# Kernel tuning notes

Measured on AMD Instinct MI355X. Metric: run time of the kernel, lower is better.

The kernel has to match this reference:

```python
import jax, jax.numpy as jnp
import numpy as np

B, T, V, H, L = 2048, 128, 256, 20, 15  # batch, seq_len, vocab, hidden, max_label


def setup_inputs() -> dict:
    key = jax.random.key(0)
    ks = jax.random.split(key, 8)
    g = lambda k, shape, s: (jax.random.normal(k, shape, jnp.float32) * s)
    return {
        "x": jax.random.randint(ks[0], (B, T), 0, V, dtype=jnp.int32),
        "W0": g(ks[1], (V, 3 * H), 0.06),   # input kernel layer 0 [V, 3H] (z|r|h)
        "U0": g(ks[2], (H, 3 * H), 0.2),    # recurrent kernel layer 0
        "b0i": jnp.zeros((3 * H,), jnp.float32),  # input bias (reset_after=True split bias)
        "b0r": jnp.zeros((3 * H,), jnp.float32),  # recurrent bias
        "W1": g(ks[3], (H, 3 * H), 0.2),
        "U1": g(ks[4], (H, 3 * H), 0.2),
        "b1i": jnp.zeros((3 * H,), jnp.float32),
        "b1r": jnp.zeros((3 * H,), jnp.float32),
        "Wd": g(ks[5], (H, L), 0.2),
        "bd": jnp.zeros((L,), jnp.float32),
        "drop_rate": 0,  # identity dropout (deterministic reference)
    }


def _gru_cell(h, xw, U, br):
    # Keras GRUCell with reset_after=True:
    #   xw = x @ W + b_in  (precomputed), rec = h @ U + b_rec
    rec = h @ U + br
    xz, xr, xh = jnp.split(xw, 3, axis=-1)
    rz, rr, rh = jnp.split(rec, 3, axis=-1)
    z = jax.nn.sigmoid(xz + rz)
    r = jax.nn.sigmoid(xr + rr)
    hh = jnp.tanh(xh + r * rh)
    return z * h + (1.0 - z) * hh


def reference(x, W0, U0, b0i, b0r, W1, U1, b1i, b1r, Wd, bd, drop_rate):
    # one_hot(x) @ W0 == gather rows of W0 (same math, no [B,T,V] materialization)
    xW0 = W0[x] + b0i                 # [B, T, 3H]
    xW0 = jnp.swapaxes(xW0, 0, 1)     # [T, B, 3H] for scan over time

    def step(carry, xw_t):
        h0, h1 = carry
        h0 = _gru_cell(h0, xw_t, U0, b0r)
        xw1 = h0 @ W1 + b1i
        h1 = _gru_cell(h1, xw1, U1, b1r)
        return (h0, h1), None

    h0 = jnp.zeros((x.shape[0], H), W0.dtype)
    h1 = jnp.zeros((x.shape[0], H), W0.dtype)
    (h0, h1), _ = jax.lax.scan(step, (h0, h1), xW0)
    # tf.nn.dropout with rate 0 is the identity
    out = h1
    logits = jax.nn.softmax(out @ Wd + bd, axis=-1)  # [B, L]
    return logits
```

## Files before the change

### kernel.cpp

```cpp
#include <hip/hip_runtime.h>


#define BB 2048
#define TT 128
#define HH 20
#define LL 15
#define H3 60

typedef float v2f __attribute__((ext_vector_type(2)));

__device__ __forceinline__ float bclane(float v, int k) {
    return __int_as_float(__builtin_amdgcn_readlane(__float_as_int(v), k));
}
__device__ __forceinline__ float dpp_rshr1(float v) {
    return __int_as_float(__builtin_amdgcn_update_dpp(
        0, __float_as_int(v), 0x111, 0xF, 0xF, true));
}
__device__ __forceinline__ float fast_rcp(float x) { return __builtin_amdgcn_rcpf(x); }
__device__ __forceinline__ float sigm(float x) { return fast_rcp(1.f + __expf(-x)); }
__device__ __forceinline__ float tanh_f(float x) { return 1.f - 2.f * fast_rcp(1.f + __expf(2.f * x)); }
#define PIN(v) asm volatile("" : "+v"(v))
#define LDSFENCE() asm volatile("" ::: "memory")

extern "C" __global__ __launch_bounds__(256)
__attribute__((amdgpu_waves_per_eu(2, 2)))
void gru2_kernel(const int* __restrict__ x, const float* __restrict__ W0,
                 const float* __restrict__ U0, const float* __restrict__ b0i,
                 const float* __restrict__ b0r, const float* __restrict__ W1,
                 const float* __restrict__ U1, const float* __restrict__ b1i,
                 const float* __restrict__ b1r, const float* __restrict__ Wd,
                 const float* __restrict__ bd, float* __restrict__ out)
{
    const int lane = threadIdx.x & 63;
    const int w = threadIdx.x >> 6;
    const int b = blockIdx.x * 4 + w;
    const int row = lane >> 4;
    const int pos = lane & 15;
    const int pc  = (pos < 15) ? pos : 14;
    const int u   = pc / 3;
    const int p3  = pc % 3;
    const int j   = row * 5 + u;
    const bool home = (pos < 15) && (p3 == 2);
    const int col = p3 * 20 + j;

    __shared__ __align__(16) float hbuf[4][2][24];
    float* h0buf = &hbuf[w][0][0];
    float* h1buf = &hbuf[w][1][0];
    if (home) { h0buf[j] = 0.f; h1buf[j] = 0.f; }
    LDSFENCE();

    v2f u0p[10], w1p[10], u1p[10];
#pragma unroll
    for (int q = 0; q < 10; ++q) {
        const int k0 = (2 * q) * H3, k1 = (2 * q + 1) * H3;
        u0p[q] = v2f{U0[k0 + col], U0[k1 + col]};
        w1p[q] = v2f{W1[k0 + col], W1[k1 + col]};
        u1p[q] = v2f{U1[k0 + col], U1[k1 + col]};
    }
#pragma unroll
    for (int q = 0; q < 10; ++q) { PIN(u0p[q]); PIN(w1p[q]); PIN(u1p[q]); }
    float bi0 = b0i[col], br0 = b0r[col], bi1 = b1i[col], br1 = b1r[col];
    PIN(bi0); PIN(br0); PIN(bi1); PIN(br1);

    const int* xrow = x + b * TT;
    const int tokA = xrow[lane];
    const int tokB = xrow[64 + lane];

    float h0 = 0.f, h1 = 0.f;

    const int tok0 = __builtin_amdgcn_readlane(tokA, 0);
    const int tok1 = __builtin_amdgcn_readlane(tokA, 1);
    int tokn2 = __builtin_amdgcn_readlane(tokA, 2);
    float xw_cur = W0[tok0 * H3 + col] + bi0;
    float xw_nxt = W0[tok1 * H3 + col];

    {
        const float pf = W0[tokn2 * H3 + col];
        const int tokn3 = __builtin_amdgcn_readlane(tokA, 3);
        const float rec0 = br0;
        const float sg0 = sigm(xw_cur + rec0);
        const float rv0 = dpp_rshr1(sg0);
        const float zv0 = dpp_rshr1(rv0);
        const float hh0 = tanh_f(xw_cur + rv0 * rec0);
        h0 = fmaf(zv0, h0 - hh0, hh0);
        if (home) h0buf[j] = h0;
        LDSFENCE();
        xw_cur = xw_nxt + bi0; xw_nxt = pf; tokn2 = tokn3;
    }

#pragma unroll 2
    for (int i = 1; i < TT; ++i) {
        const int t3 = (i + 3 < TT) ? (i + 3) : (TT - 1);
        const float pf = W0[tokn2 * H3 + col];
        const int tokn3 = __builtin_amdgcn_readlane(t3 < 64 ? tokA : tokB, t3 & 63);

        const float4* h0q = (const float4*)h0buf;
        const float4* h1q = (const float4*)h1buf;
        v2f a0 = v2f{br0, 0.f};
        v2f a1 = v2f{bi1, 0.f};
        v2f a2 = v2f{br1, 0.f};
#pragma unroll
        for (int q = 0; q < 5; ++q) {
            const float4 hv0 = h0q[q];
            const float4 hv1 = h1q[q];
            const v2f hA = v2f{hv0.x, hv0.y}, hB = v2f{hv0.z, hv0.w};
            const v2f gA = v2f{hv1.x, hv1.y}, gB = v2f{hv1.z, hv1.w};
            a0 = __builtin_elementwise_fma(hA, u0p[2 * q], a0);
            a0 = __builtin_elementwise_fma(hB, u0p[2 * q + 1], a0);
            a1 = __builtin_elementwise_fma(hA, w1p[2 * q], a1);
            a1 = __builtin_elementwise_fma(hB, w1p[2 * q + 1], a1);
            a2 = __builtin_elementwise_fma(gA, u1p[2 * q], a2);
            a2 = __builtin_elementwise_fma(gB, u1p[2 * q + 1], a2);
        }
        const float rec0 = a0.x + a0.y;
        const float xw1  = a1.x + a1.y;
        const float rec1 = a2.x + a2.y;

        const float sg0 = sigm(xw_cur + rec0);
        const float rv0 = dpp_rshr1(sg0);
        const float zv0 = dpp_rshr1(rv0);
        const float hh0 = tanh_f(xw_cur + rv0 * rec0);
        h0 = fmaf(zv0, h0 - hh0, hh0);
        if (home) h0buf[j] = h0;
        LDSFENCE();

        const float sg1 = sigm(xw1 + rec1);
        const float rv1 = dpp_rshr1(sg1);
        const float zv1 = dpp_rshr1(rv1);
        const float hh1 = tanh_f(xw1 + rv1 * rec1);
        h1 = fmaf(zv1, h1 - hh1, hh1);
        if (home) h1buf[j] = h1;
        LDSFENCE();

        xw_cur = xw_nxt + bi0; xw_nxt = pf; tokn2 = tokn3;
    }

    {
        const float4* h0q = (const float4*)h0buf;
        const float4* h1q = (const float4*)h1buf;
        v2f a1 = v2f{bi1, 0.f}, a2 = v2f{br1, 0.f};
#pragma unroll
        for (int q = 0; q < 5; ++q) {
            const float4 hv0 = h0q[q];
            const float4 hv1 = h1q[q];
            a1 = __builtin_elementwise_fma(v2f{hv0.x, hv0.y}, w1p[2 * q], a1);
            a1 = __builtin_elementwise_fma(v2f{hv0.z, hv0.w}, w1p[2 * q + 1], a1);
            a2 = __builtin_elementwise_fma(v2f{hv1.x, hv1.y}, u1p[2 * q], a2);
            a2 = __builtin_elementwise_fma(v2f{hv1.z, hv1.w}, u1p[2 * q + 1], a2);
        }
        const float xw1 = a1.x + a1.y, rec1 = a2.x + a2.y;
        const float sg1 = sigm(xw1 + rec1);
        const float rv1 = dpp_rshr1(sg1);
        const float zv1 = dpp_rshr1(rv1);
        const float hh1 = tanh_f(xw1 + rv1 * rec1);
        h1 = fmaf(zv1, h1 - hh1, hh1);
        if (home) h1buf[j] = h1;
        LDSFENCE();
    }

    const int l = lane < LL ? lane : LL - 1;
    float acc = bd[l];
#pragma unroll
    for (int k = 0; k < HH; ++k)
        acc = fmaf(h1buf[k], Wd[k * LL + l], acc);

    float m = acc;
#pragma unroll
    for (int i = 0; i < LL; ++i) m = fmaxf(m, bclane(acc, i));
    const float e = __expf(acc - m);
    float s = 0.f;
#pragma unroll
    for (int i = 0; i < LL; ++i) s += bclane(e, i);
    const float pr = e * fast_rcp(s);

    if (lane < LL) out[b * LL + lane] = pr;
}

extern "C" void kernel_launch(void* const* d_in, const int* in_sizes, int n_in,
                              void* d_out, int out_size, void* d_ws, size_t ws_size,
                              hipStream_t stream) {
    const int*   x   = (const int*)  d_in[0];
    const float* W0  = (const float*)d_in[1];
    const float* U0  = (const float*)d_in[2];
    const float* b0i = (const float*)d_in[3];
    const float* b0r = (const float*)d_in[4];
    const float* W1  = (const float*)d_in[5];
    const float* U1  = (const float*)d_in[6];
    const float* b1i = (const float*)d_in[7];
    const float* b1r = (const float*)d_in[8];
    const float* Wd  = (const float*)d_in[9];
    const float* bd  = (const float*)d_in[10];
    float* out = (float*)d_out;

    dim3 grid(BB / 4), block(256);
    hipLaunchKernelGGL(gru2_kernel, grid, block, 0, stream,
                       x, W0, U0, b0i, b0r, W1, U1, b1i, b1r, Wd, bd, out);
}
```

Baseline: 125.3 us.

## Process two batch rows per wavefront to interleave independent recurrences

After: 138.9 us. +10.9%, slower.

```diff
diff --git a/kernel.cpp b/kernel.cpp
--- a/kernel.cpp
+++ b/kernel.cpp
@@ -23,7 +23,7 @@
 #define LDSFENCE() asm volatile("" ::: "memory")
 
 extern "C" __global__ __launch_bounds__(256)
-__attribute__((amdgpu_waves_per_eu(2, 2)))
+__attribute__((amdgpu_waves_per_eu(1, 1)))
 void gru2_kernel(const int* __restrict__ x, const float* __restrict__ W0,
                  const float* __restrict__ U0, const float* __restrict__ b0i,
                  const float* __restrict__ b0r, const float* __restrict__ W1,
@@ -33,20 +33,22 @@
 {
     const int lane = threadIdx.x & 63;
     const int w = threadIdx.x >> 6;
-    const int b = blockIdx.x * 4 + w;
-    const int row = lane >> 4;
+    const int bA = blockIdx.x * 8 + w * 2;
+    const int bB = bA + 1;
     const int pos = lane & 15;
     const int pc  = (pos < 15) ? pos : 14;
     const int u   = pc / 3;
     const int p3  = pc % 3;
-    const int j   = row * 5 + u;
+    const int j   = (lane >> 4) * 5 + u;
     const bool home = (pos < 15) && (p3 == 2);
     const int col = p3 * 20 + j;
 
-    __shared__ __align__(16) float hbuf[4][2][24];
-    float* h0buf = &hbuf[w][0][0];
-    float* h1buf = &hbuf[w][1][0];
-    if (home) { h0buf[j] = 0.f; h1buf[j] = 0.f; }
+    __shared__ __align__(16) float hbuf[4][2][2][24];
+    float* h0A = &hbuf[w][0][0][0];  float* h1A = &hbuf[w][0][1][0];
+    float* h0B = &hbuf[w][1][0][0];  float* h1B = &hbuf[w][1][1][0];
+    const float4* h0Aq = (const float4*)h0A;  const float4* h1Aq = (const float4*)h1A;
+    const float4* h0Bq = (const float4*)h0B;  const float4* h1Bq = (const float4*)h1B;
+    if (home) { h0A[j] = 0.f; h1A[j] = 0.f; h0B[j] = 0.f; h1B[j] = 0.f; }
     LDSFENCE();
 
     v2f u0p[10], w1p[10], u1p[10];
@@ -62,118 +64,123 @@
     float bi0 = b0i[col], br0 = b0r[col], bi1 = b1i[col], br1 = b1r[col];
     PIN(bi0); PIN(br0); PIN(bi1); PIN(br1);
 
-    const int* xrow = x + b * TT;
-    const int tokA = xrow[lane];
-    const int tokB = xrow[64 + lane];
-
-    float h0 = 0.f, h1 = 0.f;
-
-    const int tok0 = __builtin_amdgcn_readlane(tokA, 0);
-    const int tok1 = __builtin_amdgcn_readlane(tokA, 1);
-    int tokn2 = __builtin_amdgcn_readlane(tokA, 2);
-    float xw_cur = W0[tok0 * H3 + col] + bi0;
-    float xw_nxt = W0[tok1 * H3 + col];
+    const int* xrA = x + bA * TT;
+    const int* xrB = x + bB * TT;
+    const int tA0 = xrA[lane], tA1 = xrA[64 + lane];
+    const int tB0 = xrB[lane], tB1 = xrB[64 + lane];
+
+    float h0a = 0.f, h1a = 0.f, h0b = 0.f, h1b = 0.f;
+    float4 c0a[5], c1a[5], c0b[5], c1b[5];
+
+    auto dot = [&](const float4* c, const v2f* wp, float bias) -> float {
+        v2f s0 = v2f{bias, 0.f}, s1 = v2f{0.f, 0.f};
+#pragma unroll
+        for (int q = 0; q < 5; ++q) {
+            s0 = __builtin_elementwise_fma(v2f{c[q].x, c[q].y}, wp[2 * q], s0);
+            s1 = __builtin_elementwise_fma(v2f{c[q].z, c[q].w}, wp[2 * q + 1], s1);
+        }
+        return (s0.x + s0.y) + (s1.x + s1.y);
+    };
+    auto gates = [&](float xw, float rec, float& h) {
+        const float sg = sigm(xw + rec);
+        const float rv = dpp_rshr1(sg);
+        const float zv = dpp_rshr1(rv);
+        const float hh = tanh_f(xw + rv * rec);
+        h = fmaf(zv, h - hh, hh);
+    };
+
+    int tka2 = __builtin_amdgcn_readlane(tA0, 2);
+    int tkb2 = __builtin_amdgcn_readlane(tB0, 2);
+    float xwa = W0[__builtin_amdgcn_readlane(tA0, 0) * H3 + col] + bi0;
+    float xwa_n = W0[__builtin_amdgcn_readlane(tA0, 1) * H3 + col];
+    float xwb = W0[__builtin_amdgcn_readlane(tB0, 0) * H3 + col] + bi0;
+    float xwb_n = W0[__builtin_amdgcn_readlane(tB0, 1) * H3 + col];
 
     {
-        const float pf = W0[tokn2 * H3 + col];
-        const int tokn3 = __builtin_amdgcn_readlane(tokA, 3);
-        const float rec0 = br0;
-        const float sg0 = sigm(xw_cur + rec0);
-        const float rv0 = dpp_rshr1(sg0);
-        const float zv0 = dpp_rshr1(rv0);
-        const float hh0 = tanh_f(xw_cur + rv0 * rec0);
-        h0 = fmaf(zv0, h0 - hh0, hh0);
-        if (home) h0buf[j] = h0;
-        LDSFENCE();
-        xw_cur = xw_nxt + bi0; xw_nxt = pf; tokn2 = tokn3;
-    }
-
-#pragma unroll 2
+        const float pfa = W0[tka2 * H3 + col];
+        const float pfb = W0[tkb2 * H3 + col];
+        gates(xwa, br0, h0a);
+        gates(xwb, br0, h0b);
+        if (home) { h0A[j] = h0a; h0B[j] = h0b; }
+        LDSFENCE();
+#pragma unroll
+        for (int q = 0; q < 5; ++q) {
+            c0a[q] = h0Aq[q]; c0b[q] = h0Bq[q];
+            c1a[q] = h1Aq[q]; c1b[q] = h1Bq[q];
+        }
+        xwa = xwa_n + bi0; xwa_n = pfa; tka2 = __builtin_amdgcn_readlane(tA0, 3);
+        xwb = xwb_n + bi0; xwb_n = pfb; tkb2 = __builtin_amdgcn_readlane(tB0, 3);
+    }
+
     for (int i = 1; i < TT; ++i) {
         const int t3 = (i + 3 < TT) ? (i + 3) : (TT - 1);
-        const float pf = W0[tokn2 * H3 + col];
-        const int tokn3 = __builtin_amdgcn_readlane(t3 < 64 ? tokA : tokB, t3 & 63);
-
-        const float4* h0q = (const float4*)h0buf;
-        const float4* h1q = (const float4*)h1buf;
-        v2f a0 = v2f{br0, 0.f};
-        v2f a1 = v2f{bi1, 0.f};
-        v2f a2 = v2f{br1, 0.f};
-#pragma unroll
-        for (int q = 0; q < 5; ++q) {
-            const float4 hv0 = h0q[q];
-            const float4 hv1 = h1q[q];
-            const v2f hA = v2f{hv0.x, hv0.y}, hB = v2f{hv0.z, hv0.w};
-            const v2f gA = v2f{hv1.x, hv1.y}, gB = v2f{hv1.z, hv1.w};
-            a0 = __builtin_elementwise_fma(hA, u0p[2 * q], a0);
-            a0 = __builtin_elementwise_fma(hB, u0p[2 * q + 1], a0);
-            a1 = __builtin_elementwise_fma(hA, w1p[2 * q], a1);
-            a1 = __builtin_elementwise_fma(hB, w1p[2 * q + 1], a1);
-            a2 = __builtin_elementwise_fma(gA, u1p[2 * q], a2);
-            a2 = __builtin_elementwise_fma(gB, u1p[2 * q + 1], a2);
-        }
-        const float rec0 = a0.x + a0.y;
-        const float xw1  = a1.x + a1.y;
-        const float rec1 = a2.x + a2.y;
-
-        const float sg0 = sigm(xw_cur + rec0);
-        const float rv0 = dpp_rshr1(sg0);
-        const float zv0 = dpp_rshr1(rv0);
-        const float hh0 = tanh_f(xw_cur + rv0 * rec0);
-        h0 = fmaf(zv0, h0 - hh0, hh0);
-        if (home) h0buf[j] = h0;
-        LDSFENCE();
-
-        const float sg1 = sigm(xw1 + rec1);
-        const float rv1 = dpp_rshr1(sg1);
-        const float zv1 = dpp_rshr1(rv1);
-        const float hh1 = tanh_f(xw1 + rv1 * rec1);
-        h1 = fmaf(zv1, h1 - hh1, hh1);
-        if (home) h1buf[j] = h1;
-        LDSFENCE();
-
-        xw_cur = xw_nxt + bi0; xw_nxt = pf; tokn2 = tokn3;
+        const float pfa = W0[tka2 * H3 + col];
+        const float pfb = W0[tkb2 * H3 + col];
+        const int tka3 = __builtin_amdgcn_readlane(t3 < 64 ? tA0 : tA1, t3 & 63);
+        const int tkb3 = __builtin_amdgcn_readlane(t3 < 64 ? tB0 : tB1, t3 & 63);
+
+        const float rec0a = dot(c0a, u0p, br0);
+        const float rec0b = dot(c0b, u0p, br0);
+        const float xw1a  = dot(c0a, w1p, bi1);
+        const float xw1b  = dot(c0b, w1p, bi1);
+        const float rec1a = dot(c1a, u1p, br1);
+        const float rec1b = dot(c1b, u1p, br1);
+
+        gates(xwa, rec0a, h0a);
+        gates(xwb, rec0b, h0b);
+        if (home) { h0A[j] = h0a; h0B[j] = h0b; }
+        LDSFENCE();
+#pragma unroll
+        for (int q = 0; q < 5; ++q) { c0a[q] = h0Aq[q]; c0b[q] = h0Bq[q]; }
+
+        gates(xw1a, rec1a, h1a);
+        gates(xw1b, rec1b, h1b);
+        if (home) { h1A[j] = h1a; h1B[j] = h1b; }
+        LDSFENCE();
+#pragma unroll
+        for (int q = 0; q < 5; ++q) { c1a[q] = h1Aq[q]; c1b[q] = h1Bq[q]; }
+
+        xwa = xwa_n + bi0; xwa_n = pfa; tka2 = tka3;
+        xwb = xwb_n + bi0; xwb_n = pfb; tkb2 = tkb3;
     }
 
     {
-        const float4* h0q = (const float4*)h0buf;
-        const float4* h1q = (const float4*)h1buf;
-        v2f a1 = v2f{bi1, 0.f}, a2 = v2f{br1, 0.f};
-#pragma unroll
-        for (int q = 0; q < 5; ++q) {
-            const float4 hv0 = h0q[q];
-            const float4 hv1 = h1q[q];
-            a1 = __builtin_elementwise_fma(v2f{hv0.x, hv0.y}, w1p[2 * q], a1);
-            a1 = __builtin_elementwise_fma(v2f{hv0.z, hv0.w}, w1p[2 * q + 1], a1);
-            a2 = __builtin_elementwise_fma(v2f{hv1.x, hv1.y}, u1p[2 * q], a2);
-            a2 = __builtin_elementwise_fma(v2f{hv1.z, hv1.w}, u1p[2 * q + 1], a2);
-        }
-        const float xw1 = a1.x + a1.y, rec1 = a2.x + a2.y;
-        const float sg1 = sigm(xw1 + rec1);
-        const float rv1 = dpp_rshr1(sg1);
-        const float zv1 = dpp_rshr1(rv1);
-        const float hh1 = tanh_f(xw1 + rv1 * rec1);
-        h1 = fmaf(zv1, h1 - hh1, hh1);
-        if (home) h1buf[j] = h1;
+        const float xw1a  = dot(c0a, w1p, bi1);
+        const float xw1b  = dot(c0b, w1p, bi1);
+        const float rec1a = dot(c1a, u1p, br1);
+        const float rec1b = dot(c1b, u1p, br1);
+        gates(xw1a, rec1a, h1a);
+        gates(xw1b, rec1b, h1b);
+        if (home) { h1A[j] = h1a; h1B[j] = h1b; }
         LDSFENCE();
     }
 
     const int l = lane < LL ? lane : LL - 1;
-    float acc = bd[l];
-#pragma unroll
-    for (int k = 0; k < HH; ++k)
-        acc = fmaf(h1buf[k], Wd[k * LL + l], acc);
-
-    float m = acc;
-#pragma unroll
-    for (int i = 0; i < LL; ++i) m = fmaxf(m, bclane(acc, i));
-    const float e = __expf(acc - m);
-    float s = 0.f;
-#pragma unroll
-    for (int i = 0; i < LL; ++i) s += bclane(e, i);
-    const float pr = e * fast_rcp(s);
-
-    if (lane < LL) out[b * LL + lane] = pr;
+    float accA = bd[l], accB = accA;
+#pragma unroll
+    for (int k = 0; k < HH; ++k) {
+        const float wd = Wd[k * LL + l];
+        accA = fmaf(h1A[k], wd, accA);
+        accB = fmaf(h1B[k], wd, accB);
+    }
+    float mA = accA, mB = accB;
+#pragma unroll
+    for (int i = 0; i < LL; ++i) {
+        mA = fmaxf(mA, bclane(accA, i));
+        mB = fmaxf(mB, bclane(accB, i));
+    }
+    const float eA = __expf(accA - mA);
+    const float eB = __expf(accB - mB);
+    float sA = 0.f, sB = 0.f;
+#pragma unroll
+    for (int i = 0; i < LL; ++i) {
+        sA += bclane(eA, i);
+        sB += bclane(eB, i);
+    }
+    if (lane < LL) {
+        out[bA * LL + lane] = eA * fast_rcp(sA);
+        out[bB * LL + lane] = eB * fast_rcp(sB);
+    }
 }
 
 extern "C" void kernel_launch(void* const* d_in, const int* in_sizes, int n_in,
@@ -192,7 +199,7 @@
     const float* bd  = (const float*)d_in[10];
     float* out = (float*)d_out;
 
-    dim3 grid(BB / 4), block(256);
+    dim3 grid(BB / 8), block(256);
     hipLaunchKernelGGL(gru2_kernel, grid, block, 0, stream,
                        x, W0, U0, b0i, b0r, W1, U1, b1i, b1r, Wd, bd, out);
 }
```

## Split GRU layers across separate wavefronts with block-level layer pipelining

Applied to the files above, without the earlier changes.

Result: slower. 140.8 us (+12.4%).

```diff
diff --git a/kernel.cpp b/kernel.cpp
--- a/kernel.cpp
+++ b/kernel.cpp
@@ -22,8 +22,8 @@
 #define PIN(v) asm volatile("" : "+v"(v))
 #define LDSFENCE() asm volatile("" ::: "memory")
 
-extern "C" __global__ __launch_bounds__(256)
-__attribute__((amdgpu_waves_per_eu(2, 2)))
+extern "C" __global__ __launch_bounds__(512)
+__attribute__((amdgpu_waves_per_eu(4, 4)))
 void gru2_kernel(const int* __restrict__ x, const float* __restrict__ W0,
                  const float* __restrict__ U0, const float* __restrict__ b0i,
                  const float* __restrict__ b0r, const float* __restrict__ W1,
@@ -32,148 +32,129 @@
                  const float* __restrict__ bd, float* __restrict__ out)
 {
     const int lane = threadIdx.x & 63;
-    const int w = threadIdx.x >> 6;
-    const int b = blockIdx.x * 4 + w;
-    const int row = lane >> 4;
+    const int wv = threadIdx.x >> 6;
+    const bool isL1 = (wv >= 4);
+    const int wb = wv & 3;
+    const int b = blockIdx.x * 4 + wb;
+
     const int pos = lane & 15;
     const int pc  = (pos < 15) ? pos : 14;
     const int u   = pc / 3;
     const int p3  = pc % 3;
-    const int j   = row * 5 + u;
+    const int j   = (lane >> 4) * 5 + u;
     const bool home = (pos < 15) && (p3 == 2);
     const int col = p3 * 20 + j;
 
-    __shared__ __align__(16) float hbuf[4][2][24];
-    float* h0buf = &hbuf[w][0][0];
-    float* h1buf = &hbuf[w][1][0];
-    if (home) { h0buf[j] = 0.f; h1buf[j] = 0.f; }
-    LDSFENCE();
+    __shared__ __align__(16) float h0x[4][2][24];
+    __shared__ __align__(16) float h1s[4][24];
+    if (home) { h0x[wb][0][j] = 0.f; h0x[wb][1][j] = 0.f; h1s[wb][j] = 0.f; }
+    __syncthreads();
 
-    v2f u0p[10], w1p[10], u1p[10];
+    const float* MA = isL1 ? W1 : U0;
+    const float* MB = isL1 ? U1 : U0;
+    v2f wA[10], wB[10];
 #pragma unroll
     for (int q = 0; q < 10; ++q) {
         const int k0 = (2 * q) * H3, k1 = (2 * q + 1) * H3;
-        u0p[q] = v2f{U0[k0 + col], U0[k1 + col]};
-        w1p[q] = v2f{W1[k0 + col], W1[k1 + col]};
-        u1p[q] = v2f{U1[k0 + col], U1[k1 + col]};
+        wA[q] = v2f{MA[k0 + col], MA[k1 + col]};
+        wB[q] = v2f{MB[k0 + col], MB[k1 + col]};
     }
 #pragma unroll
-    for (int q = 0; q < 10; ++q) { PIN(u0p[q]); PIN(w1p[q]); PIN(u1p[q]); }
-    float bi0 = b0i[col], br0 = b0r[col], bi1 = b1i[col], br1 = b1r[col];
-    PIN(bi0); PIN(br0); PIN(bi1); PIN(br1);
+    for (int q = 0; q < 10; ++q) { PIN(wA[q]); PIN(wB[q]); }
+    const float dbA = isL1 ? b1i[col] : b0r[col];
+    const float dbB = isL1 ? b1r[col] : 0.f;
+    const float bi0c = b0i[col];
 
     const int* xrow = x + b * TT;
-    const int tokA = xrow[lane];
-    const int tokB = xrow[64 + lane];
+    int tokA = 0, tokB = 0, tokn2 = 0;
+    float xw_cur = 0.f, xw_nxt = 0.f;
+    if (!isL1) {
+        tokA = xrow[lane];
+        tokB = xrow[64 + lane];
+        const int tok0 = __builtin_amdgcn_readlane(tokA, 0);
+        const int tok1 = __builtin_amdgcn_readlane(tokA, 1);
+        tokn2 = __builtin_amdgcn_readlane(tokA, 2);
+        xw_cur = W0[tok0 * H3 + col] + bi0c;
+        xw_nxt = W0[tok1 * H3 + col];
+    }
 
     float h0 = 0.f, h1 = 0.f;
 
-    const int tok0 = __builtin_amdgcn_readlane(tokA, 0);
-    const int tok1 = __builtin_amdgcn_readlane(tokA, 1);
-    int tokn2 = __builtin_amdgcn_readlane(tokA, 2);
-    float xw_cur = W0[tok0 * H3 + col] + bi0;
-    float xw_nxt = W0[tok1 * H3 + col];
+    for (int i = 0; i <= TT; ++i) {
+        if (!isL1) {
+            if (i < TT) {
+                const int t3 = (i + 3 < TT) ? (i + 3) : (TT - 1);
+                const float pf = W0[tokn2 * H3 + col];
+                const int tokn3 =
+                    __builtin_amdgcn_readlane(t3 < 64 ? tokA : tokB, t3 & 63);
 
-    {
-        const float pf = W0[tokn2 * H3 + col];
-        const int tokn3 = __builtin_amdgcn_readlane(tokA, 3);
-        const float rec0 = br0;
-        const float sg0 = sigm(xw_cur + rec0);
-        const float rv0 = dpp_rshr1(sg0);
-        const float zv0 = dpp_rshr1(rv0);
-        const float hh0 = tanh_f(xw_cur + rv0 * rec0);
-        h0 = fmaf(zv0, h0 - hh0, hh0);
-        if (home) h0buf[j] = h0;
-        LDSFENCE();
-        xw_cur = xw_nxt + bi0; xw_nxt = pf; tokn2 = tokn3;
+                const float4* hq = (const float4*)&h0x[wb][(i + 1) & 1][0];
+                v2f a0 = v2f{dbA, 0.f};
+#pragma unroll
+                for (int q = 0; q < 5; ++q) {
+                    const float4 hv = hq[q];
+                    a0 = __builtin_elementwise_fma(v2f{hv.x, hv.y}, wA[2 * q], a0);
+                    a0 = __builtin_elementwise_fma(v2f{hv.z, hv.w}, wA[2 * q + 1], a0);
+                }
+                const float rec0 = a0.x + a0.y;
+
+                const float sg0 = sigm(xw_cur + rec0);
+                const float rv0 = dpp_rshr1(sg0);
+                const float zv0 = dpp_rshr1(rv0);
+                const float hh0 = tanh_f(xw_cur + rv0 * rec0);
+                h0 = fmaf(zv0, h0 - hh0, hh0);
+                if (home) h0x[wb][i & 1][j] = h0;
+                LDSFENCE();
+
+                xw_cur = xw_nxt + bi0c; xw_nxt = pf; tokn2 = tokn3;
+            }
+        } else {
+            if (i >= 1) {
+                const float4* hq = (const float4*)&h0x[wb][(i + 1) & 1][0];
+                const float4* gq = (const float4*)&h1s[wb][0];
+                v2f a1 = v2f{dbA, 0.f}, a2 = v2f{dbB, 0.f};
+#pragma unroll
+                for (int q = 0; q < 5; ++q) {
+                    const float4 hv = hq[q];
+                    const float4 gv = gq[q];
+                    a1 = __builtin_elementwise_fma(v2f{hv.x, hv.y}, wA[2 * q], a1);
+                    a1 = __builtin_elementwise_fma(v2f{hv.z, hv.w}, wA[2 * q + 1], a1);
+                    a2 = __builtin_elementwise_fma(v2f{gv.x, gv.y}, wB[2 * q], a2);
+                    a2 = __builtin_elementwise_fma(v2f{gv.z, gv.w}, wB[2 * q + 1], a2);
+                }
+                const float xw1 = a1.x + a1.y;
+                const float rec1 = a2.x + a2.y;
+
+                const float sg1 = sigm(xw1 + rec1);
+                const float rv1 = dpp_rshr1(sg1);
+                const float zv1 = dpp_rshr1(rv1);
+                const float hh1 = tanh_f(xw1 + rv1 * rec1);
+                h1 = fmaf(zv1, h1 - hh1, hh1);
+                if (home) h1s[wb][j] = h1;
+                LDSFENCE();
+            }
+        }
+        __syncthreads();
     }
 
-#pragma unroll 2
-    for (int i = 1; i < TT; ++i) {
-        const int t3 = (i + 3 < TT) ? (i + 3) : (TT - 1);
-        const float pf = W0[tokn2 * H3 + col];
-        const int tokn3 = __builtin_amdgcn_readlane(t3 < 64 ? tokA : tokB, t3 & 63);
+    if (isL1) {
+        const int l = lane < LL ? lane : LL - 1;
+        float acc = bd[l];
+#pragma unroll
+        for (int k = 0; k < HH; ++k)
+            acc = fmaf(h1s[wb][k], Wd[k * LL + l], acc);
 
-        const float4* h0q = (const float4*)h0buf;
-        const float4* h1q = (const float4*)h1buf;
-        v2f a0 = v2f{br0, 0.f};
-        v2f a1 = v2f{bi1, 0.f};
-        v2f a2 = v2f{br1, 0.f};
+        float m = acc;
 #pragma unroll
-        for (int q = 0; q < 5; ++q) {
-            const float4 hv0 = h0q[q];
-            const float4 hv1 = h1q[q];
-            const v2f hA = v2f{hv0.x, hv0.y}, hB = v2f{hv0.z, hv0.w};
-            const v2f gA = v2f{hv1.x, hv1.y}, gB = v2f{hv1.z, hv1.w};
-            a0 = __builtin_elementwise_fma(hA, u0p[2 * q], a0);
-            a0 = __builtin_elementwise_fma(hB, u0p[2 * q + 1], a0);
-            a1 = __builtin_elementwise_fma(hA, w1p[2 * q], a1);
-            a1 = __builtin_elementwise_fma(hB, w1p[2 * q + 1], a1);
-            a2 = __builtin_elementwise_fma(gA, u1p[2 * q], a2);
-            a2 = __builtin_elementwise_fma(gB, u1p[2 * q + 1], a2);
-        }
-        const float rec0 = a0.x + a0.y;
-        const float xw1  = a1.x + a1.y;
-        const float rec1 = a2.x + a2.y;
+        for (int i = 0; i < LL; ++i) m = fmaxf(m, bclane(acc, i));
+        const float e = __expf(acc - m);
+        float s = 0.f;
+#pragma unroll
+        for (int i = 0; i < LL; ++i) s += bclane(e, i);
+        const float pr = e * fast_rcp(s);
 
-        const float sg0 = sigm(xw_cur + rec0);
-        const float rv0 = dpp_rshr1(sg0);
-        const float zv0 = dpp_rshr1(rv0);
-        const float hh0 = tanh_f(xw_cur + rv0 * rec0);
-        h0 = fmaf(zv0, h0 - hh0, hh0);
-        if (home) h0buf[j] = h0;
-        LDSFENCE();
-
-        const float sg1 = sigm(xw1 + rec1);
-        const float rv1 = dpp_rshr1(sg1);
-        const float zv1 = dpp_rshr1(rv1);
-        const float hh1 = tanh_f(xw1 + rv1 * rec1);
-        h1 = fmaf(zv1, h1 - hh1, hh1);
-        if (home) h1buf[j] = h1;
-        LDSFENCE();
-
-        xw_cur = xw_nxt + bi0; xw_nxt = pf; tokn2 = tokn3;
+        if (lane < LL) out[b * LL + lane] = pr;
     }
-
-    {
-        const float4* h0q = (const float4*)h0buf;
-        const float4* h1q = (const float4*)h1buf;
-        v2f a1 = v2f{bi1, 0.f}, a2 = v2f{br1, 0.f};
-#pragma unroll
-        for (int q = 0; q < 5; ++q) {
-            const float4 hv0 = h0q[q];
-            const float4 hv1 = h1q[q];
-            a1 = __builtin_elementwise_fma(v2f{hv0.x, hv0.y}, w1p[2 * q], a1);
-            a1 = __builtin_elementwise_fma(v2f{hv0.z, hv0.w}, w1p[2 * q + 1], a1);
-            a2 = __builtin_elementwise_fma(v2f{hv1.x, hv1.y}, u1p[2 * q], a2);
-            a2 = __builtin_elementwise_fma(v2f{hv1.z, hv1.w}, u1p[2 * q + 1], a2);
-        }
-        const float xw1 = a1.x + a1.y, rec1 = a2.x + a2.y;
-        const float sg1 = sigm(xw1 + rec1);
-        const float rv1 = dpp_rshr1(sg1);
-        const float zv1 = dpp_rshr1(rv1);
-        const float hh1 = tanh_f(xw1 + rv1 * rec1);
-        h1 = fmaf(zv1, h1 - hh1, hh1);
-        if (home) h1buf[j] = h1;
-        LDSFENCE();
-    }
-
-    const int l = lane < LL ? lane : LL - 1;
-    float acc = bd[l];
-#pragma unroll
-    for (int k = 0; k < HH; ++k)
-        acc = fmaf(h1buf[k], Wd[k * LL + l], acc);
-
-    float m = acc;
-#pragma unroll
-    for (int i = 0; i < LL; ++i) m = fmaxf(m, bclane(acc, i));
-    const float e = __expf(acc - m);
-    float s = 0.f;
-#pragma unroll
-    for (int i = 0; i < LL; ++i) s += bclane(e, i);
-    const float pr = e * fast_rcp(s);
-
-    if (lane < LL) out[b * LL + lane] = pr;
 }
 
 extern "C" void kernel_launch(void* const* d_in, const int* in_sizes, int n_in,
@@ -192,7 +173,7 @@
     const float* bd  = (const float*)d_in[10];
     float* out = (float*)d_out;
 
-    dim3 grid(BB / 4), block(256);
+    dim3 grid(BB / 4), block(512);
     hipLaunchKernelGGL(gru2_kernel, grid, block, 0, stream,
                        x, W0, U0, b0i, b0r, W1, U1, b1i, b1r, Wd, bd, out);
 }
```
